# Kernel optimization log

Hardware: AMD Instinct MI355X
Metric: run time of the kernel (lower is better)

## Reference

```python
import jax, jax.numpy as jnp
import numpy as np

N_QUBITS = 4
Q_LAYERS = 3
BATCH = 16384


def setup_inputs() -> dict:
    key = jax.random.key(0)
    ks = jax.random.split(key, 12)

    def n(k, shape, s=0.1):
        return (s * jax.random.normal(k, shape)).astype(jnp.float32)

    return {
        "x": jax.random.normal(ks[0], (BATCH, 1, 28, 28), jnp.float32),
        "conv1_w": n(ks[1], (6, 1, 5, 5)),
        "conv1_b": n(ks[2], (6,)),
        "conv2_w": n(ks[3], (16, 6, 5, 5)),
        "conv2_b": n(ks[4], (16,)),
        "fc1_w": n(ks[5], (120, 256)),
        "fc1_b": n(ks[6], (120,)),
        "fc2_w": n(ks[7], (N_QUBITS, 120)),
        "fc2_b": n(ks[8], (N_QUBITS,)),
        "q_weights": n(ks[9], (Q_LAYERS, 1, N_QUBITS, 3), 0.01),
        "clf_w": n(ks[10], (10, N_QUBITS)),
        "clf_b": n(ks[11], (10,)),
    }


def _apply_1q(state, U, w):
    # state: (B, 2,2,2,2); U: (2,2) shared or (B,2,2) per-sample
    s = jnp.moveaxis(state, 1 + w, -1)
    if U.ndim == 2:
        s = jnp.einsum('ij,...j->...i', U, s)
    else:
        s = jnp.einsum('bij,b...j->b...i', U, s)
    return jnp.moveaxis(s, -1, 1 + w)


def _cnot(state, c, t):
    s = jnp.moveaxis(state, (1 + c, 1 + t), (-2, -1))
    s = jnp.concatenate([s[..., 0:1, :], s[..., 1:2, ::-1]], axis=-2)
    return jnp.moveaxis(s, (-2, -1), (1 + c, 1 + t))


def _rot(phi, theta, omega):
    # PennyLane Rot = RZ(omega) @ RY(theta) @ RZ(phi)
    c = jnp.cos(theta / 2)
    s = jnp.sin(theta / 2)
    m00 = jnp.exp(-0.5j * (phi + omega)) * c
    m01 = -jnp.exp(0.5j * (phi - omega)) * s
    m10 = jnp.exp(0.5j * (omega - phi)) * s
    m11 = jnp.exp(0.5j * (phi + omega)) * c
    return jnp.stack([jnp.stack([m00, m01]), jnp.stack([m10, m11])])


def _rx(a):
    # a: (B,) -> (B,2,2) RX matrices
    c = jnp.cos(a / 2) + 0j
    z = -1j * jnp.sin(a / 2)
    return jnp.stack([jnp.stack([c, z], -1), jnp.stack([z, c], -1)], -2)


def _circuit(angles, qw):
    # Data-reuploading circuit: per block, StronglyEntanglingLayers(1 sublayer, r=1)
    # then AngleEmbedding (RX). Returns <Z_i> per qubit, shape (B, 4).
    Bn = angles.shape[0]
    state = jnp.zeros((Bn, 16), jnp.complex64).at[:, 0].set(1.0)
    state = state.reshape(Bn, 2, 2, 2, 2)
    n_layers = qw.shape[0]
    for l in range(n_layers):
        for w in range(N_QUBITS):
            state = _apply_1q(state, _rot(qw[l, 0, w, 0], qw[l, 0, w, 1], qw[l, 0, w, 2]), w)
        for w in range(N_QUBITS):
            state = _cnot(state, w, (w + 1) % N_QUBITS)
        for w in range(N_QUBITS):
            state = _apply_1q(state, _rx(angles[:, w]), w)
    probs = jnp.abs(state) ** 2
    z = []
    for w in range(N_QUBITS):
        p = jnp.moveaxis(probs, 1 + w, -1).reshape(Bn, -1, 2)
        z.append(p[..., 0].sum(-1) - p[..., 1].sum(-1))
    return jnp.stack(z, axis=1).astype(jnp.float32)


def _conv(x, w, b):
    y = jax.lax.conv_general_dilated(x, w, (1, 1), 'VALID',
                                     dimension_numbers=('NCHW', 'OIHW', 'NCHW'))
    return y + b[None, :, None, None]


def _pool(x):
    return jax.lax.reduce_window(x, -jnp.inf, jax.lax.max,
                                 (1, 1, 2, 2), (1, 1, 2, 2), 'VALID')


def reference(x, conv1_w, conv1_b, conv2_w, conv2_b, fc1_w, fc1_b,
              fc2_w, fc2_b, q_weights, clf_w, clf_b):
    h = _pool(jax.nn.relu(_conv(x, conv1_w, conv1_b)))       # (B,6,12,12)
    h = _pool(jax.nn.relu(_conv(h, conv2_w, conv2_b)))       # (B,16,4,4)
    h = h.reshape(h.shape[0], -1)                            # (B,256)
    h = jax.nn.relu(h @ fc1_w.T + fc1_b)                     # (B,120)
    feat = h @ fc2_w.T + fc2_b                               # (B,4)
    angles = jnp.pi * jax.nn.sigmoid(feat)
    q_out = _circuit(angles, q_weights)                      # (B,4)
    logits = q_out @ clf_w.T + clf_b                         # (B,10)
    return logits
```

## Files before the change

### kernel.cpp

```cpp
#include <hip/hip_runtime.h>
#include <math.h>

#define BATCH_N 16384

typedef _Float16 half8 __attribute__((ext_vector_type(8)));
typedef __fp16 h2 __attribute__((ext_vector_type(2)));
typedef float f32x4 __attribute__((ext_vector_type(4)));

#define C1P_F  0
#define BS1_F  120
#define BS2_F  128
#define FC2W_F 144
#define ROTM_F 628
#define RXCS_F 724
#define CWB_F  788
#define W2B_F  840
#define PW_F   2696
#define LDS_FLOATS 7688

__global__ __launch_bounds__(256, 5) void fused_model(
    const float* __restrict__ xg,
    const float* __restrict__ c1w, const float* __restrict__ c1b,
    const float* __restrict__ c2w, const float* __restrict__ c2b,
    const float* __restrict__ f1w, const float* __restrict__ f1b,
    const float* __restrict__ f2w, const float* __restrict__ f2b,
    const float* __restrict__ qw,  const float* __restrict__ cw,
    const float* __restrict__ cbias, float* __restrict__ out) {
    __shared__ float L[LDS_FLOATS];
    const int tid = threadIdx.x;
    const int b0 = blockIdx.x * 8;
    const int lane = tid & 63, wvi = tid >> 6;
    const int ml = lane & 15, q = lane >> 4;

    _Float16* W2BH = (_Float16*)(L + W2B_F);
    _Float16* PWH  = (_Float16*)(L + PW_F);
    _Float16* H1CH = PWH + wvi * 2496;
    _Float16* HSH  = PWH + 512;

    if (tid < 120) {
        const int oc = tid / 20, r = tid - oc * 20, ky = r >> 2, j = r & 3;
        const float* wb = c1w + oc * 25 + ky * 5;
        float lo, hi;
        if (j == 0)      { lo = wb[0]; hi = wb[1]; }
        else if (j == 1) { lo = wb[2]; hi = wb[3]; }
        else if (j == 2) { lo = wb[4]; hi = 0.f;   }
        else             { lo = 0.f;   hi = wb[4]; }
        ((h2*)&L[C1P_F])[tid] = __builtin_amdgcn_cvt_pkrtz(lo, hi);
    }
    if (tid < 6)  L[BS1_F + tid] = c1b[tid];
    if (tid < 16) L[BS2_F + tid] = c2b[tid];
    for (int i = tid; i < 480; i += 256) L[FC2W_F + i] = f2w[i];
    if (tid < 4) L[FC2W_F + 480 + tid] = f2b[tid];
    if (tid < 40) L[CWB_F + tid] = cw[tid];
    if (tid < 10) L[CWB_F + 40 + tid] = cbias[tid];
    if (tid < 12) {
        const float phi = qw[tid * 3 + 0];
        const float th  = qw[tid * 3 + 1];
        const float om  = qw[tid * 3 + 2];
        const float ct = cosf(0.5f * th), st = sinf(0.5f * th);
        const float ap = 0.5f * (phi + om), bm = 0.5f * (phi - om);
        const float ca = cosf(ap), sa = sinf(ap);
        const float cbm = cosf(bm), sbm = sinf(bm);
        float* R = &L[ROTM_F + tid * 8];
        R[0] =  ct * ca;  R[1] = -ct * sa;
        R[2] = -st * cbm; R[3] = -st * sbm;
        R[4] =  st * cbm; R[5] = -st * sbm;
        R[6] =  ct * ca;  R[7] =  ct * sa;
    }
    for (int i = tid; i < 3712; i += 256) {
        const int oc = i / 232, r = i - oc * 232;
        float v = 0.f;
        if (r < 200) {
            const int pix = r >> 3, ic = r & 7;
            if (ic < 6) v = c2w[oc * 150 + ic * 25 + pix];
        }
        W2BH[oc * 232 + r] = (_Float16)v;
    }
    __syncthreads();

    for (int t = lane; t < 288; t += 64) {
        const int s = t >= 144 ? 1 : 0;
        const int r = t - s * 144;
        const int py = r / 12, px = r - (r / 12) * 12;
        const float* xp = xg + (size_t)(b0 + 2 * wvi + s) * 784 + (2 * py) * 28 + 2 * px;

        float4 X4[6]; float2 X2[6];
#pragma unroll
        for (int rr = 0; rr < 6; rr++) {
            X4[rr] = *(const float4*)(xp + rr * 28);
            X2[rr] = *(const float2*)(xp + rr * 28 + 4);
        }

        float acc[6][4];
#pragma unroll
        for (int oc = 0; oc < 6; oc++) {
            const float bv = L[BS1_F + oc];
            acc[oc][0] = bv; acc[oc][1] = bv; acc[oc][2] = bv; acc[oc][3] = bv;
        }

        h2 R0[5], R1[5];
        R0[0] = __builtin_amdgcn_cvt_pkrtz(X4[0].x, X4[0].y);
        R0[1] = __builtin_amdgcn_cvt_pkrtz(X4[0].z, X4[0].w);
        R0[2] = __builtin_amdgcn_cvt_pkrtz(X2[0].x, X2[0].y);
        R0[3] = __builtin_amdgcn_cvt_pkrtz(X4[0].y, X4[0].z);
        R0[4] = __builtin_amdgcn_cvt_pkrtz(X4[0].w, X2[0].x);
#pragma unroll
        for (int ky = 0; ky < 5; ky++) {
            R1[0] = __builtin_amdgcn_cvt_pkrtz(X4[ky + 1].x, X4[ky + 1].y);
            R1[1] = __builtin_amdgcn_cvt_pkrtz(X4[ky + 1].z, X4[ky + 1].w);
            R1[2] = __builtin_amdgcn_cvt_pkrtz(X2[ky + 1].x, X2[ky + 1].y);
            R1[3] = __builtin_amdgcn_cvt_pkrtz(X4[ky + 1].y, X4[ky + 1].z);
            R1[4] = __builtin_amdgcn_cvt_pkrtz(X4[ky + 1].w, X2[ky + 1].x);
#pragma unroll
            for (int oc = 0; oc < 6; oc++) {
                union { uint4 v; h2 h[4]; } W;
                W.v = ((const uint4*)&L[C1P_F])[oc * 5 + ky];
                acc[oc][0] = __builtin_amdgcn_fdot2(R0[0], W.h[0], acc[oc][0], false);
                acc[oc][0] = __builtin_amdgcn_fdot2(R0[1], W.h[1], acc[oc][0], false);
                acc[oc][0] = __builtin_amdgcn_fdot2(R0[2], W.h[2], acc[oc][0], false);
                acc[oc][1] = __builtin_amdgcn_fdot2(R0[3], W.h[0], acc[oc][1], false);
                acc[oc][1] = __builtin_amdgcn_fdot2(R0[4], W.h[1], acc[oc][1], false);
                acc[oc][1] = __builtin_amdgcn_fdot2(R0[2], W.h[3], acc[oc][1], false);
                acc[oc][2] = __builtin_amdgcn_fdot2(R1[0], W.h[0], acc[oc][2], false);
                acc[oc][2] = __builtin_amdgcn_fdot2(R1[1], W.h[1], acc[oc][2], false);
                acc[oc][2] = __builtin_amdgcn_fdot2(R1[2], W.h[2], acc[oc][2], false);
                acc[oc][3] = __builtin_amdgcn_fdot2(R1[3], W.h[0], acc[oc][3], false);
                acc[oc][3] = __builtin_amdgcn_fdot2(R1[4], W.h[1], acc[oc][3], false);
                acc[oc][3] = __builtin_amdgcn_fdot2(R1[2], W.h[3], acc[oc][3], false);
            }
#pragma unroll
            for (int j = 0; j < 5; j++) R0[j] = R1[j];
        }

        union { _Float16 h[8]; uint4 u; } O;
#pragma unroll
        for (int oc = 0; oc < 6; oc++) {
            const float m = fmaxf(fmaxf(acc[oc][0], acc[oc][1]), fmaxf(acc[oc][2], acc[oc][3]));
            O.h[oc] = (_Float16)fmaxf(m, 0.f);
        }
        O.h[6] = (_Float16)0.f; O.h[7] = (_Float16)0.f;
        *(uint4*)(H1CH + s * 1248 + (py * 13 + px) * 8) = O.u;
    }
    __builtin_amdgcn_wave_barrier();

    {
        f32x4 c2a[2][4];
#pragma unroll
        for (int a = 0; a < 2; a++)
#pragma unroll
            for (int b = 0; b < 4; b++) c2a[a][b] = (f32x4){0.f, 0.f, 0.f, 0.f};

#pragma unroll
        for (int ks = 0; ks < 7; ks++) {
            const half8 bfrag = *(const half8*)(W2BH + ml * 232 + ks * 32 + q * 8);
            int tp = ks * 4 + q; if (tp > 24) tp = 24;
            const int poff = (tp / 5) * 13 + (tp % 5);
#pragma unroll
            for (int si = 0; si < 2; si++) {
                const _Float16* hp = H1CH + si * 1248;
#pragma unroll
                for (int t = 0; t < 4; t++) {
                    const int cp = t * 16 + ml;
                    const int unit = (cp >> 3) * 13 + (cp & 7) + poff;
                    const half8 afrag = *(const half8*)(hp + unit * 8);
                    c2a[si][t] = __builtin_amdgcn_mfma_f32_16x16x32_f16(afrag, bfrag, c2a[si][t], 0, 0, 0);
                }
            }
        }

        const float bv = L[BS2_F + ml];
#pragma unroll
        for (int si = 0; si < 2; si++) {
#pragma unroll
            for (int t = 0; t < 4; t++) {
                const float c0 = c2a[si][t][0] + bv, c1 = c2a[si][t][1] + bv;
                const float c2 = c2a[si][t][2] + bv, c3 = c2a[si][t][3] + bv;
                float px0 = fmaxf(c0, c1), px1 = fmaxf(c2, c3);
                px0 = fmaxf(px0, __shfl_xor(px0, 32));
                px1 = fmaxf(px1, __shfl_xor(px1, 32));
                if (lane < 32) {
                    union { _Float16 h[2]; unsigned u; } P2;
                    P2.h[0] = (_Float16)fmaxf(px0, 0.f);
                    P2.h[1] = (_Float16)fmaxf(px1, 0.f);
                    *(unsigned*)(PWH + wvi * 2496 + si * 256 + ml * 16 + t * 4 + (q & 1) * 2) = P2.u;
                }
            }
        }
    }
    __syncthreads();

    {
        f32x4 fcC[2];
        fcC[0] = (f32x4){0.f, 0.f, 0.f, 0.f};
        fcC[1] = (f32x4){0.f, 0.f, 0.f, 0.f};
        const int ms = (ml < 8) ? ml : 0;
        const _Float16* h2p = PWH + (ms >> 1) * 2496 + (ms & 1) * 256;
#pragma unroll
        for (int ks = 0; ks < 8; ks++) {
            const half8 afrag = *(const half8*)(h2p + ks * 32 + q * 8);
#pragma unroll
            for (int ti = 0; ti < 2; ti++) {
                const int n = (wvi + 4 * ti) * 16 + ml;
                half8 bfrag;
                if (n < 120) {
                    const float* wp = f1w + (size_t)n * 256 + ks * 32 + q * 8;
                    const float4 u = *(const float4*)wp;
                    const float4 v = *(const float4*)(wp + 4);
                    bfrag[0] = (_Float16)u.x; bfrag[1] = (_Float16)u.y;
                    bfrag[2] = (_Float16)u.z; bfrag[3] = (_Float16)u.w;
                    bfrag[4] = (_Float16)v.x; bfrag[5] = (_Float16)v.y;
                    bfrag[6] = (_Float16)v.z; bfrag[7] = (_Float16)v.w;
                } else {
#pragma unroll
                    for (int j = 0; j < 8; j++) bfrag[j] = (_Float16)0.f;
                }
                fcC[ti] = __builtin_amdgcn_mfma_f32_16x16x32_f16(afrag, bfrag, fcC[ti], 0, 0, 0);
            }
        }
        if (q < 2) {
#pragma unroll
            for (int ti = 0; ti < 2; ti++) {
                const int n = (wvi + 4 * ti) * 16 + ml;
                if (n < 120) {
                    const float bb = f1b[n];
#pragma unroll
                    for (int rg = 0; rg < 4; rg++) {
                        const int s = q * 4 + rg;
                        HSH[s * 128 + n] = (_Float16)fmaxf(fcC[ti][rg] + bb, 0.f);
                    }
                }
            }
        }
    }
    __syncthreads();

    if (tid < 32) {
        const int s = tid >> 2, m = tid & 3;
        float f = L[FC2W_F + 480 + m];
        for (int nn = 0; nn < 120; nn += 8) {
            const half8 hv = *(const half8*)(HSH + s * 128 + nn);
            const float* wp = &L[FC2W_F + m * 120 + nn];
            f = fmaf(wp[0], (float)hv[0], f); f = fmaf(wp[1], (float)hv[1], f);
            f = fmaf(wp[2], (float)hv[2], f); f = fmaf(wp[3], (float)hv[3], f);
            f = fmaf(wp[4], (float)hv[4], f); f = fmaf(wp[5], (float)hv[5], f);
            f = fmaf(wp[6], (float)hv[6], f); f = fmaf(wp[7], (float)hv[7], f);
        }
        const float ang = 3.14159265358979323846f / (1.f + expf(-f));
        L[RXCS_F + tid]      = cosf(0.5f * ang);
        L[RXCS_F + 32 + tid] = sinf(0.5f * ang);
    }
    __syncthreads();

    if (tid < 128) {
        const int s = tid >> 4, a = tid & 15;
        float ar = (a == 0) ? 1.f : 0.f, ai = 0.f;

#pragma unroll
        for (int l = 0; l < 3; l++) {
#pragma unroll
            for (int w = 0; w < 4; w++) {
                const float* R = &L[ROTM_F + (l * 4 + w) * 8];
                const int mask = 8 >> w;
                const float pr = __shfl_xor(ar, mask);
                const float pi = __shfl_xor(ai, mask);
                const bool bit = (a & mask) != 0;
                const float lr = bit ? pr : ar, li = bit ? pi : ai;
                const float hr = bit ? ar : pr, hi = bit ? ai : pi;
                const float Ar = bit ? R[4] : R[0], Ai = bit ? R[5] : R[1];
                const float Br = bit ? R[6] : R[2], Bi = bit ? R[7] : R[3];
                ar = Ar * lr - Ai * li + Br * hr - Bi * hi;
                ai = Ar * li + Ai * lr + Br * hi + Bi * hr;
            }
#pragma unroll
            for (int w = 0; w < 4; w++) {
                const int mc = 8 >> w, mt = 8 >> ((w + 1) & 3);
                const float pr = __shfl_xor(ar, mt);
                const float pi = __shfl_xor(ai, mt);
                const bool ctrl = (a & mc) != 0;
                ar = ctrl ? pr : ar;
                ai = ctrl ? pi : ai;
            }
#pragma unroll
            for (int w = 0; w < 4; w++) {
                const int mask = 8 >> w;
                const float c  = L[RXCS_F + s * 4 + w];
                const float s2 = L[RXCS_F + 32 + s * 4 + w];
                const float pr = __shfl_xor(ar, mask);
                const float pi = __shfl_xor(ai, mask);
                const float nr = fmaf(c, ar, s2 * pi);
                const float ni = fmaf(c, ai, -s2 * pr);
                ar = nr; ai = ni;
            }
        }

        float v = ar * ar + ai * ai;
#pragma unroll
        for (int d = 1; d < 16; d <<= 1) {
            const float pv = __shfl_xor(v, d);
            v = (a & d) ? (pv - v) : (v + pv);
        }

        if (a < 10) {
            const int base = (tid & 63) & ~15;
            float lg = L[CWB_F + 40 + a];
#pragma unroll
            for (int w = 0; w < 4; w++) {
                const float zw = __shfl(v, base | (8 >> w));
                lg = fmaf(L[CWB_F + a * 4 + w], zw, lg);
            }
            out[(size_t)(b0 + s) * 10 + a] = lg;
        }
    }
}

extern "C" void kernel_launch(void* const* d_in, const int* in_sizes, int n_in,
                              void* d_out, int out_size, void* d_ws, size_t ws_size,
                              hipStream_t stream) {
    const float* x   = (const float*)d_in[0];
    const float* c1w = (const float*)d_in[1];
    const float* c1b = (const float*)d_in[2];
    const float* c2w = (const float*)d_in[3];
    const float* c2b = (const float*)d_in[4];
    const float* f1w = (const float*)d_in[5];
    const float* f1b = (const float*)d_in[6];
    const float* f2w = (const float*)d_in[7];
    const float* f2b = (const float*)d_in[8];
    const float* qw  = (const float*)d_in[9];
    const float* cw  = (const float*)d_in[10];
    const float* cb  = (const float*)d_in[11];
    float* out = (float*)d_out;

    fused_model<<<BATCH_N / 8, 256, 0, stream>>>(x, c1w, c1b, c2w, c2b,
                                                 f1w, f1b, f2w, f2b,
                                                 qw, cw, cb, out);
}
```

Before: 164.3 us.

## Split fused model into conv1 kernel plus rest kernel via fp16 workspace

Breaks the single fused kernel into two launches. The first computes conv1+ReLU+pool with packed fp16 dot products over many blocks, writing padded fp16 activations to the workspace, and also converts fc1 weights to fp16. The second loads those activations asynchronously into LDS and runs conv2, fc1, fc2 and the quantum circuit as before. The goal is to take conv1 off the fused kernel's critical path and give it better parallelism, at the cost of a workspace round-trip through global memory, a second launch, and a fallback path when the workspace is too small.

```diff
diff --git a/kernel.cpp b/kernel.cpp
--- a/kernel.cpp
+++ b/kernel.cpp
@@ -17,6 +17,322 @@
 #define W2B_F  840
 #define PW_F   2696
 #define LDS_FLOATS 7688
+#define B_LDS_FLOATS 7816
+
+#define H1_SAMP_H 1280
+#define F1WH_OFF_H ((size_t)BATCH_N * H1_SAMP_H)
+#define WS_NEED_BYTES (F1WH_OFF_H * 2 + (size_t)120 * 256 * 2)
+#define A_CONV_BLOCKS 2304
+#define A_TOTAL_BLOCKS (A_CONV_BLOCKS + 120)
+
+__global__ __launch_bounds__(256, 6) void conv1_k(
+    const float* __restrict__ xg, const float* __restrict__ c1w,
+    const float* __restrict__ c1b, const float* __restrict__ f1w,
+    _Float16* __restrict__ ws) {
+    const int tid = threadIdx.x;
+
+    if (blockIdx.x >= A_CONV_BLOCKS) {
+        const int idx = (blockIdx.x - A_CONV_BLOCKS) * 256 + tid;
+        ws[F1WH_OFF_H + idx] = (_Float16)f1w[idx];
+        return;
+    }
+
+    __shared__ float Lw[126];
+    if (tid < 120) {
+        const int oc = tid / 20, r = tid - oc * 20, ky = r >> 2, j = r & 3;
+        const float* wb = c1w + oc * 25 + ky * 5;
+        float lo, hi;
+        if (j == 0)      { lo = wb[0]; hi = wb[1]; }
+        else if (j == 1) { lo = wb[2]; hi = wb[3]; }
+        else if (j == 2) { lo = wb[4]; hi = 0.f;   }
+        else             { lo = 0.f;   hi = wb[4]; }
+        ((h2*)Lw)[tid] = __builtin_amdgcn_cvt_pkrtz(lo, hi);
+    }
+    if (tid < 6) Lw[120 + tid] = c1b[tid];
+    __syncthreads();
+
+#pragma unroll 1
+    for (int u = 0; u < 4; u++) {
+        const int i = blockIdx.x * 1024 + u * 256 + tid;
+        const int s = i / 144;
+        const int r = i - s * 144;
+        const int py = r / 12;
+        const int px = r - py * 12;
+        const float* xp = xg + (size_t)s * 784 + py * 56 + px * 2;
+
+        h2 R[6][5];
+#pragma unroll
+        for (int rr = 0; rr < 6; rr++) {
+            const float4 a = *(const float4*)(xp + rr * 28);
+            const float2 c = *(const float2*)(xp + rr * 28 + 4);
+            R[rr][0] = __builtin_amdgcn_cvt_pkrtz(a.x, a.y);
+            R[rr][1] = __builtin_amdgcn_cvt_pkrtz(a.z, a.w);
+            R[rr][2] = __builtin_amdgcn_cvt_pkrtz(c.x, c.y);
+            R[rr][3] = __builtin_amdgcn_cvt_pkrtz(a.y, a.z);
+            R[rr][4] = __builtin_amdgcn_cvt_pkrtz(a.w, c.x);
+        }
+
+        float acc[6][4];
+#pragma unroll
+        for (int oc = 0; oc < 6; oc++) {
+            const float bv = Lw[120 + oc];
+            acc[oc][0] = bv; acc[oc][1] = bv; acc[oc][2] = bv; acc[oc][3] = bv;
+        }
+#pragma unroll
+        for (int ky = 0; ky < 5; ky++) {
+#pragma unroll
+            for (int oc = 0; oc < 6; oc++) {
+                union { uint4 v; h2 h[4]; } W;
+                W.v = ((const uint4*)Lw)[oc * 5 + ky];
+                acc[oc][0] = __builtin_amdgcn_fdot2(R[ky][0], W.h[0], acc[oc][0], false);
+                acc[oc][0] = __builtin_amdgcn_fdot2(R[ky][1], W.h[1], acc[oc][0], false);
+                acc[oc][0] = __builtin_amdgcn_fdot2(R[ky][2], W.h[2], acc[oc][0], false);
+                acc[oc][1] = __builtin_amdgcn_fdot2(R[ky][3], W.h[0], acc[oc][1], false);
+                acc[oc][1] = __builtin_amdgcn_fdot2(R[ky][4], W.h[1], acc[oc][1], false);
+                acc[oc][1] = __builtin_amdgcn_fdot2(R[ky][2], W.h[3], acc[oc][1], false);
+                acc[oc][2] = __builtin_amdgcn_fdot2(R[ky + 1][0], W.h[0], acc[oc][2], false);
+                acc[oc][2] = __builtin_amdgcn_fdot2(R[ky + 1][1], W.h[1], acc[oc][2], false);
+                acc[oc][2] = __builtin_amdgcn_fdot2(R[ky + 1][2], W.h[2], acc[oc][2], false);
+                acc[oc][3] = __builtin_amdgcn_fdot2(R[ky + 1][3], W.h[0], acc[oc][3], false);
+                acc[oc][3] = __builtin_amdgcn_fdot2(R[ky + 1][4], W.h[1], acc[oc][3], false);
+                acc[oc][3] = __builtin_amdgcn_fdot2(R[ky + 1][2], W.h[3], acc[oc][3], false);
+            }
+        }
+
+        union { _Float16 h[8]; uint4 uu; } O;
+#pragma unroll
+        for (int oc = 0; oc < 6; oc++) {
+            const float m = fmaxf(fmaxf(acc[oc][0], acc[oc][1]), fmaxf(acc[oc][2], acc[oc][3]));
+            O.h[oc] = (_Float16)fmaxf(m, 0.f);
+        }
+        O.h[6] = (_Float16)0.f; O.h[7] = (_Float16)0.f;
+        *(uint4*)(ws + (size_t)s * H1_SAMP_H + (py * 13 + px) * 8) = O.uu;
+    }
+}
+
+__global__ __launch_bounds__(256, 5) void rest_model(
+    const _Float16* __restrict__ h1g, const _Float16* __restrict__ f1wh,
+    const float* __restrict__ c2w, const float* __restrict__ c2b,
+    const float* __restrict__ f1b,
+    const float* __restrict__ f2w, const float* __restrict__ f2b,
+    const float* __restrict__ qw,  const float* __restrict__ cw,
+    const float* __restrict__ cbias, float* __restrict__ out) {
+    __shared__ float L[B_LDS_FLOATS];
+    const int tid = threadIdx.x;
+    const int b0 = blockIdx.x * 8;
+    const int lane = tid & 63, wvi = tid >> 6;
+    const int ml = lane & 15, q = lane >> 4;
+
+    _Float16* W2BH = (_Float16*)(L + W2B_F);
+    _Float16* PWH  = (_Float16*)(L + PW_F);
+    _Float16* H1CH = PWH + wvi * 2560;
+    _Float16* HSH  = PWH + 512;
+
+    {
+        const _Float16* src = h1g + (size_t)(b0 + 2 * wvi) * H1_SAMP_H + lane * 8;
+#pragma unroll
+        for (int it = 0; it < 5; ++it) {
+            __builtin_amdgcn_global_load_lds(
+                (const __attribute__((address_space(1))) void*)(src + it * 512),
+                (__attribute__((address_space(3))) void*)(H1CH + it * 512),
+                16, 0, 0);
+        }
+    }
+
+    if (tid < 16) L[BS2_F + tid] = c2b[tid];
+    for (int i = tid; i < 480; i += 256) L[FC2W_F + i] = f2w[i];
+    if (tid < 4) L[FC2W_F + 480 + tid] = f2b[tid];
+    if (tid < 40) L[CWB_F + tid] = cw[tid];
+    if (tid < 10) L[CWB_F + 40 + tid] = cbias[tid];
+    if (tid < 12) {
+        const float phi = qw[tid * 3 + 0];
+        const float th  = qw[tid * 3 + 1];
+        const float om  = qw[tid * 3 + 2];
+        const float ct = cosf(0.5f * th), st = sinf(0.5f * th);
+        const float ap = 0.5f * (phi + om), bm = 0.5f * (phi - om);
+        const float ca = cosf(ap), sa = sinf(ap);
+        const float cbm = cosf(bm), sbm = sinf(bm);
+        float* R = &L[ROTM_F + tid * 8];
+        R[0] =  ct * ca;  R[1] = -ct * sa;
+        R[2] = -st * cbm; R[3] = -st * sbm;
+        R[4] =  st * cbm; R[5] = -st * sbm;
+        R[6] =  ct * ca;  R[7] =  ct * sa;
+    }
+    for (int i = tid; i < 3712; i += 256) {
+        const int oc = i / 232, r = i - oc * 232;
+        float v = 0.f;
+        if (r < 200) {
+            const int pix = r >> 3, ic = r & 7;
+            if (ic < 6) v = c2w[oc * 150 + ic * 25 + pix];
+        }
+        W2BH[oc * 232 + r] = (_Float16)v;
+    }
+    __syncthreads();
+    asm volatile("s_waitcnt vmcnt(0)" ::: "memory");
+
+    {
+        f32x4 c2a[2][4];
+#pragma unroll
+        for (int a = 0; a < 2; a++)
+#pragma unroll
+            for (int b = 0; b < 4; b++) c2a[a][b] = (f32x4){0.f, 0.f, 0.f, 0.f};
+
+#pragma unroll
+        for (int ks = 0; ks < 7; ks++) {
+            const half8 bfrag = *(const half8*)(W2BH + ml * 232 + ks * 32 + q * 8);
+            int tp = ks * 4 + q; if (tp > 24) tp = 24;
+            const int poff = (tp / 5) * 13 + (tp % 5);
+#pragma unroll
+            for (int si = 0; si < 2; si++) {
+                const _Float16* hp = H1CH + si * H1_SAMP_H;
+#pragma unroll
+                for (int t = 0; t < 4; t++) {
+                    const int cp = t * 16 + ml;
+                    const int unit = (cp >> 3) * 13 + (cp & 7) + poff;
+                    const half8 afrag = *(const half8*)(hp + unit * 8);
+                    c2a[si][t] = __builtin_amdgcn_mfma_f32_16x16x32_f16(afrag, bfrag, c2a[si][t], 0, 0, 0);
+                }
+            }
+        }
+
+        const float bv = L[BS2_F + ml];
+#pragma unroll
+        for (int si = 0; si < 2; si++) {
+#pragma unroll
+            for (int t = 0; t < 4; t++) {
+                const float c0 = c2a[si][t][0] + bv, c1 = c2a[si][t][1] + bv;
+                const float c2 = c2a[si][t][2] + bv, c3 = c2a[si][t][3] + bv;
+                float px0 = fmaxf(c0, c1), px1 = fmaxf(c2, c3);
+                px0 = fmaxf(px0, __shfl_xor(px0, 32));
+                px1 = fmaxf(px1, __shfl_xor(px1, 32));
+                if (lane < 32) {
+                    union { _Float16 h[2]; unsigned u; } P2;
+                    P2.h[0] = (_Float16)fmaxf(px0, 0.f);
+                    P2.h[1] = (_Float16)fmaxf(px1, 0.f);
+                    *(unsigned*)(PWH + wvi * 2560 + si * 256 + ml * 16 + t * 4 + (q & 1) * 2) = P2.u;
+                }
+            }
+        }
+    }
+    __syncthreads();
+
+    {
+        f32x4 fcC[2];
+        fcC[0] = (f32x4){0.f, 0.f, 0.f, 0.f};
+        fcC[1] = (f32x4){0.f, 0.f, 0.f, 0.f};
+        const int ms = (ml < 8) ? ml : 0;
+        const _Float16* h2p = PWH + (ms >> 1) * 2560 + (ms & 1) * 256;
+#pragma unroll
+        for (int ks = 0; ks < 8; ks++) {
+            const half8 afrag = *(const half8*)(h2p + ks * 32 + q * 8);
+#pragma unroll
+            for (int ti = 0; ti < 2; ti++) {
+                const int n = (wvi + 4 * ti) * 16 + ml;
+                half8 bfrag;
+                if (n < 120) {
+                    bfrag = *(const half8*)(f1wh + (size_t)n * 256 + ks * 32 + q * 8);
+                } else {
+#pragma unroll
+                    for (int j = 0; j < 8; j++) bfrag[j] = (_Float16)0.f;
+                }
+                fcC[ti] = __builtin_amdgcn_mfma_f32_16x16x32_f16(afrag, bfrag, fcC[ti], 0, 0, 0);
+            }
+        }
+        if (q < 2) {
+#pragma unroll
+            for (int ti = 0; ti < 2; ti++) {
+                const int n = (wvi + 4 * ti) * 16 + ml;
+                if (n < 120) {
+                    const float bb = f1b[n];
+#pragma unroll
+                    for (int rg = 0; rg < 4; rg++) {
+                        const int s = q * 4 + rg;
+                        HSH[s * 128 + n] = (_Float16)fmaxf(fcC[ti][rg] + bb, 0.f);
+                    }
+                }
+            }
+        }
+    }
+    __syncthreads();
+
+    if (tid < 32) {
+        const int s = tid >> 2, m = tid & 3;
+        float f = L[FC2W_F + 480 + m];
+        for (int nn = 0; nn < 120; nn += 8) {
+            const half8 hv = *(const half8*)(HSH + s * 128 + nn);
+            const float* wp = &L[FC2W_F + m * 120 + nn];
+            f = fmaf(wp[0], (float)hv[0], f); f = fmaf(wp[1], (float)hv[1], f);
+            f = fmaf(wp[2], (float)hv[2], f); f = fmaf(wp[3], (float)hv[3], f);
+            f = fmaf(wp[4], (float)hv[4], f); f = fmaf(wp[5], (float)hv[5], f);
+            f = fmaf(wp[6], (float)hv[6], f); f = fmaf(wp[7], (float)hv[7], f);
+        }
+        const float ang = 3.14159265358979323846f / (1.f + expf(-f));
+        L[RXCS_F + tid]      = cosf(0.5f * ang);
+        L[RXCS_F + 32 + tid] = sinf(0.5f * ang);
+    }
+    __syncthreads();
+
+    if (tid < 128) {
+        const int s = tid >> 4, a = tid & 15;
+        float ar = (a == 0) ? 1.f : 0.f, ai = 0.f;
+
+#pragma unroll
+        for (int l = 0; l < 3; l++) {
+#pragma unroll
+            for (int w = 0; w < 4; w++) {
+                const float* R = &L[ROTM_F + (l * 4 + w) * 8];
+                const int mask = 8 >> w;
+                const float pr = __shfl_xor(ar, mask);
+                const float pi = __shfl_xor(ai, mask);
+                const bool bit = (a & mask) != 0;
+                const float lr = bit ? pr : ar, li = bit ? pi : ai;
+                const float hr = bit ? ar : pr, hi = bit ? ai : pi;
+                const float Ar = bit ? R[4] : R[0], Ai = bit ? R[5] : R[1];
+                const float Br = bit ? R[6] : R[2], Bi = bit ? R[7] : R[3];
+                ar = Ar * lr - Ai * li + Br * hr - Bi * hi;
+                ai = Ar * li + Ai * lr + Br * hi + Bi * hr;
+            }
+#pragma unroll
+            for (int w = 0; w < 4; w++) {
+                const int mc = 8 >> w, mt = 8 >> ((w + 1) & 3);
+                const float pr = __shfl_xor(ar, mt);
+                const float pi = __shfl_xor(ai, mt);
+                const bool ctrl = (a & mc) != 0;
+                ar = ctrl ? pr : ar;
+                ai = ctrl ? pi : ai;
+            }
+#pragma unroll
+            for (int w = 0; w < 4; w++) {
+                const int mask = 8 >> w;
+                const float c  = L[RXCS_F + s * 4 + w];
+                const float s2 = L[RXCS_F + 32 + s * 4 + w];
+                const float pr = __shfl_xor(ar, mask);
+                const float pi = __shfl_xor(ai, mask);
+                const float nr = fmaf(c, ar, s2 * pi);
+                const float ni = fmaf(c, ai, -s2 * pr);
+                ar = nr; ai = ni;
+            }
+        }
+
+        float v = ar * ar + ai * ai;
+#pragma unroll
+        for (int d = 1; d < 16; d <<= 1) {
+            const float pv = __shfl_xor(v, d);
+            v = (a & d) ? (pv - v) : (v + pv);
+        }
+
+        if (a < 10) {
+            const int base = (tid & 63) & ~15;
+            float lg = L[CWB_F + 40 + a];
+#pragma unroll
+            for (int w = 0; w < 4; w++) {
+                const float zw = __shfl(v, base | (8 >> w));
+                lg = fmaf(L[CWB_F + a * 4 + w], zw, lg);
+            }
+            out[(size_t)(b0 + s) * 10 + a] = lg;
+        }
+    }
+}
 
 __global__ __launch_bounds__(256, 5) void fused_model(
     const float* __restrict__ xg,
@@ -330,7 +646,15 @@
     const float* cb  = (const float*)d_in[11];
     float* out = (float*)d_out;
 
-    fused_model<<<BATCH_N / 8, 256, 0, stream>>>(x, c1w, c1b, c2w, c2b,
-                                                 f1w, f1b, f2w, f2b,
-                                                 qw, cw, cb, out);
+    if (d_ws != nullptr && ws_size >= WS_NEED_BYTES) {
+        _Float16* wsh = (_Float16*)d_ws;
+        conv1_k<<<A_TOTAL_BLOCKS, 256, 0, stream>>>(x, c1w, c1b, f1w, wsh);
+        rest_model<<<BATCH_N / 8, 256, 0, stream>>>(wsh, wsh + F1WH_OFF_H,
+                                                    c2w, c2b, f1b, f2w, f2b,
+                                                    qw, cw, cb, out);
+    } else {
+        fused_model<<<BATCH_N / 8, 256, 0, stream>>>(x, c1w, c1b, c2w, c2b,
+                                                     f1w, f1b, f2w, f2b,
+                                                     qw, cw, cb, out);
+    }
 }
```

Measured after the change: 381.8 us. +132.4%, slower.
